# Kernel optimization log

Measured on AMD Instinct MI355X. Metric: run time of the kernel, lower is better.

Reference implementation:

```python
import jax, jax.numpy as jnp
import numpy as np

VOCAB = 50257   # N_max = len(word_to_idx)
IN_DIM = 256
HID = 13        # forced: out Linear in_features = 2*hidden_dim must equal dec output 2*13
L = 2048


def _lstm_dir(seq, Wih, Whh, b, reverse):
    """Single-direction LSTM over seq [T, F] with zero init. b = b_ih + b_hh.
    Torch gate order: i, f, g, o."""
    H = Whh.shape[1]

    def step(carry, x_t):
        h, c = carry
        z = Wih @ x_t + Whh @ h + b                  # (4H,)
        i, f, g, o = jnp.split(z, 4)
        c2 = jax.nn.sigmoid(f) * c + jax.nn.sigmoid(i) * jnp.tanh(g)
        h2 = jax.nn.sigmoid(o) * jnp.tanh(c2)
        return (h2, c2), h2

    init = (jnp.zeros((H,), seq.dtype), jnp.zeros((H,), seq.dtype))
    (hn, cn), hs = jax.lax.scan(step, init, seq, reverse=reverse)
    return hs, hn, cn


def _dec_cell(x_scalar, h, c, Wih, Whh, b):
    """One LSTM cell step with scalar input (input_size=1). Returns new h."""
    z = Wih[:, 0] * x_scalar + Whh @ h + b
    i, f, g, o = jnp.split(z, 4)
    c2 = jax.nn.sigmoid(f) * c + jax.nn.sigmoid(i) * jnp.tanh(g)
    return jax.nn.sigmoid(o) * jnp.tanh(c2)


def setup_inputs() -> dict:
    key = jax.random.key(0)
    ks = jax.random.split(key, 16)
    s = 0.05
    G = 4 * HID  # 52; also num_layers*2*HID = 52 (proj in_features)
    return {
        "x": jax.random.randint(ks[0], (L,), 0, VOCAB),
        "emb_W": jax.random.normal(ks[1], (VOCAB + 1, IN_DIM)) * s,
        "enc_Wih0": jax.random.normal(ks[2], (2, G, IN_DIM)) * s,   # [dir, 4H, in]
        "enc_Whh0": jax.random.normal(ks[3], (2, G, HID)) * s,
        "enc_b0": jax.random.normal(ks[4], (2, G)) * s,
        "enc_Wih1": jax.random.normal(ks[5], (2, G, 2 * HID)) * s,  # layer1 input = 2*HID
        "enc_Whh1": jax.random.normal(ks[6], (2, G, HID)) * s,
        "enc_b1": jax.random.normal(ks[7], (2, G)) * s,
        "proj1_W": jax.random.normal(ks[8], (2 * HID, 2 * 2 * HID)) * s,
        "proj1_b": jax.random.normal(ks[9], (2 * HID,)) * s,
        "proj2_W": jax.random.normal(ks[10], (2 * HID, 2 * 2 * HID)) * s,
        "proj2_b": jax.random.normal(ks[11], (2 * HID,)) * s,
        "dec_Wih": jax.random.normal(ks[12], (2, G, 1)) * s,
        "dec_Whh": jax.random.normal(ks[13], (2, G, HID)) * s,
        "dec_b": jax.random.normal(ks[14], (2, G)) * s,
        "out_W": jax.random.normal(ks[15], (VOCAB, 2 * HID)) * s,
        "out_b": jnp.zeros((VOCAB,), jnp.float32),
    }


def reference(x, emb_W, enc_Wih0, enc_Whh0, enc_b0, enc_Wih1, enc_Whh1, enc_b1,
              proj1_W, proj1_b, proj2_W, proj2_b, dec_Wih, dec_Whh, dec_b,
              out_W, out_b):
    embs = emb_W[x]                                            # (L, IN_DIM)

    # Encoder: 2-layer bidirectional LSTM, batch=1 (vectors).
    hs_f0, hnf0, cnf0 = _lstm_dir(embs, enc_Wih0[0], enc_Whh0[0], enc_b0[0], False)
    hs_b0, hnb0, cnb0 = _lstm_dir(embs, enc_Wih0[1], enc_Whh0[1], enc_b0[1], True)
    out0 = jnp.concatenate([hs_f0, hs_b0], axis=-1)            # (L, 2*HID)
    _, hnf1, cnf1 = _lstm_dir(out0, enc_Wih1[0], enc_Whh1[0], enc_b1[0], False)
    _, hnb1, cnb1 = _lstm_dir(out0, enc_Wih1[1], enc_Whh1[1], enc_b1[1], True)

    # torch h_n layout: [l0_fwd, l0_bwd, l1_fwd, l1_bwd]
    h_flat = jnp.concatenate([hnf0, hnb0, hnf1, hnb1])         # (52,)
    c_flat = jnp.concatenate([cnf0, cnb0, cnf1, cnb1])
    state_h = (proj1_W @ h_flat + proj1_b).reshape(2, HID)     # dec (dir, HID) init
    state_c = (proj2_W @ c_flat + proj2_b).reshape(2, HID)

    # Decoder step 0: input -1.0 with projected initial state.
    start = jnp.float32(-1.0)
    step0 = jnp.concatenate([
        _dec_cell(start, state_h[0], state_c[0], dec_Wih[0], dec_Whh[0], dec_b[0]),
        _dec_cell(start, state_h[1], state_c[1], dec_Wih[1], dec_Whh[1], dec_b[1]),
    ])                                                          # (26,)

    # Steps i>0: original code calls self.dec(input) with NO hidden state, so each
    # step uses zero initial state and depends only on x[i-1] -> fully parallel.
    xs = x[:-1].astype(jnp.float32)                             # (L-1,)
    z0 = jnp.zeros((HID,), jnp.float32)
    rest = jax.vmap(lambda v: jnp.concatenate([
        _dec_cell(v, z0, z0, dec_Wih[0], dec_Whh[0], dec_b[0]),
        _dec_cell(v, z0, z0, dec_Wih[1], dec_Whh[1], dec_b[1]),
    ]))(xs)                                                     # (L-1, 26)

    dec_out = jnp.concatenate([step0[None, :], rest], axis=0)   # (L, 26)
    preds = dec_out @ out_W.T + out_b                           # (L, VOCAB)
    return preds, embs
```

## Files before the change

kernel.cpp:

```cpp
#include <hip/hip_runtime.h>
#include <hip/hip_bf16.h>
#include <cstdint>
#include <cstddef>

#define L      2048
#define IN_DIM 256
#define HID    13
#define G      52
#define VOCAB  50257
#define PRED_N ((size_t)L * VOCAB)
#define L2E    1.4426950408889634f
#define INV2L2E 0.34657359027997264f
#define NTX    99
#define NTY    16
#define NTILE  (NTX * NTY)

static __device__ __forceinline__ float fexp2(float x) { return __builtin_amdgcn_exp2f(x); }
static __device__ __forceinline__ float frcp(float x) { return __builtin_amdgcn_rcpf(x); }
static __device__ __forceinline__ float sigm(float z) { return 1.f - frcp(fexp2(z * L2E) + 1.f); }
static __device__ __forceinline__ float tanh_(float z) { return 1.f - 2.f * frcp(fexp2(z * (2.f * L2E)) + 1.f); }
static __device__ __forceinline__ float bcast(float v, int l) {
    return __int_as_float(__builtin_amdgcn_readlane(__float_as_int(v), l));
}

__global__ void k_emb_u0(const int* __restrict__ x, const float* __restrict__ embW,
                         const float* __restrict__ Wih0, const float* __restrict__ b0,
                         float* __restrict__ out_embs, float* __restrict__ u0)
{
    __shared__ float se[IN_DIM];
    int t = blockIdx.x;
    int tid = threadIdx.x;
    int rowx = x[t];
    float2 e = ((const float2*)(embW + (size_t)rowx * IN_DIM))[tid];
    se[2 * tid]     = e.x;
    se[2 * tid + 1] = e.y;
    ((float2*)(out_embs + (size_t)t * IN_DIM))[tid] = e;
    __syncthreads();
    if (tid < 2 * G) {
        int dirg = tid / G, g = tid % G;
        int gate = g / HID, row = g % HID;
        float msc = (gate == 2) ? 2.f * L2E : L2E;
        float acc = b0[dirg * G + g];
        const float* w = Wih0 + (size_t)(dirg * G + g) * IN_DIM;
        #pragma unroll 8
        for (int k = 0; k < IN_DIM; ++k)
            acc = fmaf(w[k], se[k], acc);
        u0[((size_t)dirg * L + t) * 64 + gate * 16 + row] = msc * acc;
    } else {
        int p = tid - 2 * G;
        int dirp = p / 12, pp = p % 12;
        int gate = pp / 3, row = HID + pp % 3;
        u0[((size_t)dirp * L + t) * 64 + gate * 16 + row] = 0.f;
    }
}

__global__ void k_rest(const int* __restrict__ x, const float* __restrict__ dWih,
                       const float* __restrict__ db, float* __restrict__ dec)
{
    int idx = blockIdx.x * blockDim.x + threadIdx.x;
    if (idx >= (L - 1) * 2 * HID) return;
    int i = idx / (2 * HID) + 1;
    int j = idx % (2 * HID);
    int dir = j / HID, jj = j % HID;
    float v = (float)x[i - 1];
    int base = dir * G;
    float zi = fmaf(dWih[base + jj],           v, db[base + jj]);
    float zg = fmaf(dWih[base + 2 * HID + jj], v, db[base + 2 * HID + jj]);
    float zo = fmaf(dWih[base + 3 * HID + jj], v, db[base + 3 * HID + jj]);
    float c2 = sigm(zi) * tanh_(zg);
    dec[(size_t)i * (2 * HID) + j] = sigm(zo) * tanh_(c2);
}

template<bool DOUT>
static __device__ __forceinline__ void chain_run(
    const float* __restrict__ ub, int pstep,
    const float* __restrict__ whh, float kcv, float onev,
    bool m16, bool m32,
    float* __restrict__ outp,
    float& hout, float& cout)
{
    float h = 0.f, c = 0.f;
    float cur[8], nxt[8];
    #pragma unroll
    for (int k = 0; k < 8; ++k) cur[k] = ub[k * pstep];
    #pragma unroll
    for (int k = 0; k < 8; ++k) nxt[k] = cur[k];
    const float* upf = ub + (ptrdiff_t)8 * pstep;

    for (int tcb = 0; tcb < L; tcb += 8) {
        if (tcb + 8 < L) {
            #pragma unroll
            for (int k = 0; k < 8; ++k) nxt[k] = upf[k * pstep];
            upf += (ptrdiff_t)8 * pstep;
        }
        #pragma unroll
        for (int k = 0; k < 8; ++k) {
            float h0 = bcast(h, 0), h1 = bcast(h, 1), h2 = bcast(h, 2), h3 = bcast(h, 3);
            float h4 = bcast(h, 4), h5 = bcast(h, 5), h6 = bcast(h, 6), h7 = bcast(h, 7);
            float h8 = bcast(h, 8), h9 = bcast(h, 9), h10 = bcast(h, 10), h11 = bcast(h, 11);
            float h12 = bcast(h, 12);
            float A = fmaf(whh[0], h0, cur[k]);
            float B = whh[1] * h1;
            float C = whh[2] * h2;
            float D = whh[3] * h3;
            A = fmaf(whh[4], h4, A);   B = fmaf(whh[5], h5, B);
            C = fmaf(whh[6], h6, C);   D = fmaf(whh[7], h7, D);
            A = fmaf(whh[8], h8, A);   B = fmaf(whh[9], h9, B);
            C = fmaf(whh[10], h10, C); D = fmaf(whh[11], h11, D);
            A = fmaf(whh[12], h12, A);
            float z = (A + B) + (C + D);
            float act = fmaf(-kcv, frcp(fexp2(z) + 1.f), onev);
            float pa = act, pb = act;
            asm("s_nop 1\n\tv_permlane16_swap_b32 %0, %1" : "+v"(pa), "+v"(pb));
            float sf = m16 ? pa : pb;
            float qa = act, qb = act;
            asm("s_nop 1\n\tv_permlane32_swap_b32 %0, %1" : "+v"(qa), "+v"(qb));
            float tg = m32 ? qa : qb;
            float ra = tg, rb = tg;
            asm("s_nop 1\n\tv_permlane16_swap_b32 %0, %1" : "+v"(ra), "+v"(rb));
            float so = m16 ? ra : rb;
            float c2 = fmaf(sf, c, act * tg);
            float th = fmaf(-2.f, frcp(fexp2(c2) + 1.f), 1.f);
            h = so * th;
            c = c2;
            if (DOUT) { *outp = h; outp += pstep; }
        }
        #pragma unroll
        for (int k = 0; k < 8; ++k) cur[k] = nxt[k];
    }
    hout = h; cout = c;
}

static __device__ __forceinline__ void chain_setup_and_run(
    const float* __restrict__ u, const float* __restrict__ Whh,
    float* __restrict__ out0p, float* __restrict__ finh, float* __restrict__ finc,
    int chain_base, int do_out0, int dir, int lane)
{
    int lg16 = lane & 15, gate = lane >> 4;
    int rsrc = gate * HID + (lg16 < HID ? lg16 : HID - 1);
    float kcv, onev;
    if (gate == 2)      { kcv = 2.f;        onev = 1.f; }
    else if (gate == 0) { kcv = 2.f * L2E;  onev = 2.f * L2E; }
    else                { kcv = 1.f;        onev = 1.f; }
    float msc = (gate == 2) ? 2.f * L2E : L2E;
    float whh[HID];
    #pragma unroll
    for (int k = 0; k < HID; ++k) whh[k] = msc * Whh[(dir * G + rsrc) * HID + k];

    int ia = lane, ib = lane;
    asm("s_nop 1\n\tv_permlane16_swap_b32 %0, %1" : "+v"(ia), "+v"(ib));
    bool m16 = (ia == (lane ^ 16));
    int ja = lane, jb = lane;
    asm("s_nop 1\n\tv_permlane32_swap_b32 %0, %1" : "+v"(ja), "+v"(jb));
    bool m32 = (ja == (lane ^ 32));

    const float* ub = u + (size_t)dir * L * 64 + (dir ? (size_t)(L - 1) * 64 : 0) + lane;
    int pstep = dir ? -64 : 64;
    float* outp = out0p + ((size_t)dir * L + (dir ? L - 1 : 0)) * 64 + lane;

    float h, c;
    if (do_out0) chain_run<true >(ub, pstep, whh, kcv, onev, m16, m32, outp, h, c);
    else         chain_run<false>(ub, pstep, whh, kcv, onev, m16, m32, outp, h, c);

    if (lane < HID) {
        finh[(chain_base + dir) * HID + lane] = h;
        finc[(chain_base + dir) * HID + lane] = c * INV2L2E;
    }
}

__global__ void __launch_bounds__(256) k_phase0(
    const float* __restrict__ u, const float* __restrict__ Whh,
    float* __restrict__ out0p, float* __restrict__ finh, float* __restrict__ finc,
    const float* __restrict__ dec, const float* __restrict__ outW,
    const float* __restrict__ outb, float* __restrict__ preds)
{
    __shared__ float sd[128][28];
    int bid = blockIdx.x;
    int tid = threadIdx.x;
    if (bid >= 2) {
        __builtin_amdgcn_s_setprio(0);
        int tile = bid - 2;
        int ix = tile % NTX, iy = tile / NTX;
        int nbase = ix * 512, i0 = iy * 128;
        for (int li = tid; li < 128 * 26; li += 256) {
            int r = li / 26, cc = li % 26;
            sd[r][cc] = dec[(size_t)(i0 + r) * 26 + cc];
        }
        __syncthreads();
        int n0 = nbase + tid, n1 = nbase + 256 + tid;
        bool a0 = n0 < VOCAB, a1 = n1 < VOCAB;
        float w0[26], w1[26], b0v = 0.f, b1v = 0.f;
        #pragma unroll
        for (int k = 0; k < 26; ++k) { w0[k] = 0.f; w1[k] = 0.f; }
        if (a0) { const float* w = outW + (size_t)n0 * 26;
            #pragma unroll
            for (int k = 0; k < 26; ++k) w0[k] = w[k];
            b0v = outb[n0]; }
        if (a1) { const float* w = outW + (size_t)n1 * 26;
            #pragma unroll
            for (int k = 0; k < 26; ++k) w1[k] = w[k];
            b1v = outb[n1]; }
        for (int i = 0; i < 128; ++i) {
            int grow = i0 + i;
            float acc0 = b0v, acc1 = b1v;
            const float* dr = sd[i];
            #pragma unroll
            for (int k = 0; k < 26; ++k) {
                float d = dr[k];
                acc0 = fmaf(d, w0[k], acc0);
                acc1 = fmaf(d, w1[k], acc1);
            }
            if (grow != 0) {
                size_t rb = (size_t)grow * VOCAB;
                if (a0) preds[rb + n0] = acc0;
                if (a1) preds[rb + n1] = acc1;
            }
        }
        return;
    }
    if (tid >= 64) return;
    __builtin_amdgcn_s_setprio(3);
    chain_setup_and_run(u, Whh, out0p, finh, finc, 0, 1, bid, tid);
}

__global__ void __launch_bounds__(64) k_phase1(
    const float* __restrict__ u, const float* __restrict__ Whh,
    float* __restrict__ finh, float* __restrict__ finc)
{
    chain_setup_and_run(u, Whh, (float*)nullptr, finh, finc, 2, 0, blockIdx.x, threadIdx.x);
}

__global__ void k_u1(const float* __restrict__ out0p, const float* __restrict__ Wih1,
                     const float* __restrict__ b1, float* __restrict__ u1)
{
    int idx = blockIdx.x * blockDim.x + threadIdx.x;
    if (idx >= L * 2 * 64) return;
    int t    = idx >> 7;
    int remv = idx & 127;
    int d1   = remv >> 6;
    int lane = remv & 63;
    int gate = lane >> 4, row = lane & 15;
    size_t oidx = ((size_t)d1 * L + t) * 64 + lane;
    if (row >= HID) { u1[oidx] = 0.f; return; }
    int g = gate * HID + row;
    float msc = (gate == 2) ? 2.f * L2E : L2E;
    float acc = b1[d1 * G + g];
    const float* w = Wih1 + (size_t)(d1 * G + g) * (2 * HID);
    const float* o0 = out0p + (size_t)t * 64;
    const float* o1 = out0p + ((size_t)L + t) * 64;
    #pragma unroll
    for (int k = 0; k < HID; ++k)
        acc = fmaf(w[k], o0[k], acc);
    #pragma unroll
    for (int k = 0; k < HID; ++k)
        acc = fmaf(w[HID + k], o1[k], acc);
    u1[oidx] = msc * acc;
}

__global__ void __launch_bounds__(64) k_final(const float* __restrict__ fin_h, const float* __restrict__ fin_c,
                                              const float* __restrict__ p1W, const float* __restrict__ p1b,
                                              const float* __restrict__ p2W, const float* __restrict__ p2b,
                                              const float* __restrict__ dWih, const float* __restrict__ dWhh,
                                              const float* __restrict__ db, float* __restrict__ dec)
{
    __shared__ float sh[2 * HID], sc[2 * HID], sz[G];
    int tid = threadIdx.x;
    if (tid < 4 * HID) {
        int r = tid < 2 * HID ? tid : tid - 2 * HID;
        const float* W   = tid < 2 * HID ? p1W : p2W;
        const float* src = tid < 2 * HID ? fin_h : fin_c;
        float acc = tid < 2 * HID ? p1b[r] : p2b[r];
        for (int k = 0; k < 4 * HID; ++k) acc = fmaf(W[r * 4 * HID + k], src[k], acc);
        if (tid < 2 * HID) sh[r] = acc; else sc[r] = acc;
    }
    __syncthreads();
    for (int dir = 0; dir < 2; ++dir) {
        if (tid < G) {
            float acc = db[dir * G + tid] - dWih[dir * G + tid];
            for (int k = 0; k < HID; ++k)
                acc = fmaf(dWhh[(dir * G + tid) * HID + k], sh[dir * HID + k], acc);
            sz[tid] = acc;
        }
        __syncthreads();
        if (tid < HID) {
            float si = sigm(sz[tid]);
            float sf = sigm(sz[HID + tid]);
            float tg = tanh_(sz[2 * HID + tid]);
            float so = sigm(sz[3 * HID + tid]);
            float c2 = fmaf(sf, sc[dir * HID + tid], si * tg);
            dec[dir * HID + tid] = so * tanh_(c2);
        }
        __syncthreads();
    }
}

__global__ void k_row0(const float* __restrict__ dec, const float* __restrict__ outW,
                       const float* __restrict__ outb, float* __restrict__ preds)
{
    int n = blockIdx.x * blockDim.x + threadIdx.x;
    if (n >= VOCAB) return;
    float acc = outb[n];
    const float* w = outW + (size_t)n * 26;
    #pragma unroll
    for (int k = 0; k < 26; ++k) acc = fmaf(w[k], dec[k], acc);
    preds[n] = acc;
}

extern "C" void kernel_launch(void* const* d_in, const int* in_sizes, int n_in,
                              void* d_out, int out_size, void* d_ws, size_t ws_size,
                              hipStream_t stream)
{
    (void)in_sizes; (void)n_in; (void)out_size; (void)ws_size;

    const int*   x     = (const int*)d_in[0];
    const float* embW  = (const float*)d_in[1];
    const float* eWih0 = (const float*)d_in[2];
    const float* eWhh0 = (const float*)d_in[3];
    const float* eb0   = (const float*)d_in[4];
    const float* eWih1 = (const float*)d_in[5];
    const float* eWhh1 = (const float*)d_in[6];
    const float* eb1   = (const float*)d_in[7];
    const float* p1W   = (const float*)d_in[8];
    const float* p1b   = (const float*)d_in[9];
    const float* p2W   = (const float*)d_in[10];
    const float* p2b   = (const float*)d_in[11];
    const float* dWih  = (const float*)d_in[12];
    const float* dWhh  = (const float*)d_in[13];
    const float* db    = (const float*)d_in[14];
    const float* outW  = (const float*)d_in[15];
    const float* outb  = (const float*)d_in[16];

    float* ws    = (float*)d_ws;
    float* u0    = ws;
    float* u1    = u0 + 2 * L * 64;
    float* out0p = u1 + 2 * L * 64;
    float* dec   = out0p + 2 * L * 64;
    float* fin_h = dec + L * 2 * HID;
    float* fin_c = fin_h + G;

    float* preds    = (float*)d_out;
    float* out_embs = preds + PRED_N;

    hipLaunchKernelGGL(k_emb_u0, dim3(L), dim3(128), 0, stream,
                       x, embW, eWih0, eb0, out_embs, u0);

    int restN = (L - 1) * 2 * HID;
    hipLaunchKernelGGL(k_rest, dim3((restN + 255) / 256), dim3(256), 0, stream, x, dWih, db, dec);

    hipLaunchKernelGGL(k_phase0, dim3(2 + NTILE), dim3(256), 0, stream,
                       u0, eWhh0, out0p, fin_h, fin_c,
                       dec, outW, outb, preds);

    hipLaunchKernelGGL(k_u1, dim3((L * 2 * 64 + 255) / 256), dim3(256), 0, stream,
                       out0p, eWih1, eb1, u1);

    hipLaunchKernelGGL(k_phase1, dim3(2), dim3(64), 0, stream,
                       u1, eWhh1, fin_h, fin_c);

    hipLaunchKernelGGL(k_final, dim3(1), dim3(64), 0, stream,
                       fin_h, fin_c, p1W, p1b, p2W, p2b, dWih, dWhh, db, dec);

    hipLaunchKernelGGL(k_row0, dim3((VOCAB + 255) / 256), dim3(256), 0, stream,
                       dec, outW, outb, preds);
}
```

Before: 611.3 us.

## Fuse decoder rest kernel into embedding kernel and persist GEMM tiles over fewer blocks

Moves the per-timestep decoder cell computation into the embedding/u0 kernel by adding 32 extra threads per block, which removes one kernel launch. The output-projection blocks in phase0 become persistent: 254 blocks each loop over a contiguous range of tiles instead of launching one block per tile. This is meant to cut launch and block scheduling overhead and leave CUs free for the latency-bound recurrent chains. The risk is reduced parallelism for the large prediction write and some load imbalance between blocks. It also adds a stray, harmless redefinition of PRED_N.

```diff
diff --git a/kernel.cpp b/kernel.cpp
--- a/kernel.cpp
+++ b/kernel.cpp
@@ -8,12 +8,15 @@
 #define HID    13
 #define G      52
 #define VOCAB  50257
-#define PRED_N ((size_t)L * VOCAB)
+#define PRED_N ((size_t)L * VOOCAB)
 #define L2E    1.4426950408889634f
 #define INV2L2E 0.34657359027997264f
 #define NTX    99
 #define NTY    16
 #define NTILE  (NTX * NTY)
+#define GB     254
+#undef PRED_N
+#define PRED_N ((size_t)L * VOCAB)
 
 static __device__ __forceinline__ float fexp2(float x) { return __builtin_amdgcn_exp2f(x); }
 static __device__ __forceinline__ float frcp(float x) { return __builtin_amdgcn_rcpf(x); }
@@ -23,18 +26,22 @@
     return __int_as_float(__builtin_amdgcn_readlane(__float_as_int(v), l));
 }
 
-__global__ void k_emb_u0(const int* __restrict__ x, const float* __restrict__ embW,
-                         const float* __restrict__ Wih0, const float* __restrict__ b0,
-                         float* __restrict__ out_embs, float* __restrict__ u0)
+__global__ void __launch_bounds__(160) k_emb_u0(
+    const int* __restrict__ x, const float* __restrict__ embW,
+    const float* __restrict__ Wih0, const float* __restrict__ b0,
+    const float* __restrict__ dWih, const float* __restrict__ db,
+    float* __restrict__ out_embs, float* __restrict__ u0, float* __restrict__ dec)
 {
     __shared__ float se[IN_DIM];
     int t = blockIdx.x;
     int tid = threadIdx.x;
-    int rowx = x[t];
-    float2 e = ((const float2*)(embW + (size_t)rowx * IN_DIM))[tid];
-    se[2 * tid]     = e.x;
-    se[2 * tid + 1] = e.y;
-    ((float2*)(out_embs + (size_t)t * IN_DIM))[tid] = e;
+    if (tid < 128) {
+        int rowx = x[t];
+        float2 e = ((const float2*)(embW + (size_t)rowx * IN_DIM))[tid];
+        se[2 * tid]     = e.x;
+        se[2 * tid + 1] = e.y;
+        ((float2*)(out_embs + (size_t)t * IN_DIM))[tid] = e;
+    }
     __syncthreads();
     if (tid < 2 * G) {
         int dirg = tid / G, g = tid % G;
@@ -46,29 +53,22 @@
         for (int k = 0; k < IN_DIM; ++k)
             acc = fmaf(w[k], se[k], acc);
         u0[((size_t)dirg * L + t) * 64 + gate * 16 + row] = msc * acc;
-    } else {
+    } else if (tid < 128) {
         int p = tid - 2 * G;
         int dirp = p / 12, pp = p % 12;
         int gate = pp / 3, row = HID + pp % 3;
         u0[((size_t)dirp * L + t) * 64 + gate * 16 + row] = 0.f;
-    }
-}
-
-__global__ void k_rest(const int* __restrict__ x, const float* __restrict__ dWih,
-                       const float* __restrict__ db, float* __restrict__ dec)
-{
-    int idx = blockIdx.x * blockDim.x + threadIdx.x;
-    if (idx >= (L - 1) * 2 * HID) return;
-    int i = idx / (2 * HID) + 1;
-    int j = idx % (2 * HID);
-    int dir = j / HID, jj = j % HID;
-    float v = (float)x[i - 1];
-    int base = dir * G;
-    float zi = fmaf(dWih[base + jj],           v, db[base + jj]);
-    float zg = fmaf(dWih[base + 2 * HID + jj], v, db[base + 2 * HID + jj]);
-    float zo = fmaf(dWih[base + 3 * HID + jj], v, db[base + 3 * HID + jj]);
-    float c2 = sigm(zi) * tanh_(zg);
-    dec[(size_t)i * (2 * HID) + j] = sigm(zo) * tanh_(c2);
+    } else if (tid < 128 + 2 * HID && t >= 1) {
+        int j = tid - 128;
+        int dir = j / HID, jj = j % HID;
+        float v = (float)x[t - 1];
+        int base = dir * G;
+        float zi = fmaf(dWih[base + jj],           v, db[base + jj]);
+        float zg = fmaf(dWih[base + 2 * HID + jj], v, db[base + 2 * HID + jj]);
+        float zo = fmaf(dWih[base + 3 * HID + jj], v, db[base + 3 * HID + jj]);
+        float c2 = sigm(zi) * tanh_(zg);
+        dec[(size_t)t * (2 * HID) + j] = sigm(zo) * tanh_(c2);
+    }
 }
 
 template<bool DOUT>
@@ -179,41 +179,48 @@
     int tid = threadIdx.x;
     if (bid >= 2) {
         __builtin_amdgcn_s_setprio(0);
-        int tile = bid - 2;
-        int ix = tile % NTX, iy = tile / NTX;
-        int nbase = ix * 512, i0 = iy * 128;
-        for (int li = tid; li < 128 * 26; li += 256) {
-            int r = li / 26, cc = li % 26;
-            sd[r][cc] = dec[(size_t)(i0 + r) * 26 + cc];
-        }
-        __syncthreads();
-        int n0 = nbase + tid, n1 = nbase + 256 + tid;
-        bool a0 = n0 < VOCAB, a1 = n1 < VOCAB;
-        float w0[26], w1[26], b0v = 0.f, b1v = 0.f;
-        #pragma unroll
-        for (int k = 0; k < 26; ++k) { w0[k] = 0.f; w1[k] = 0.f; }
-        if (a0) { const float* w = outW + (size_t)n0 * 26;
+        int b = bid - 2;
+        const int q = NTILE / GB, r = NTILE % GB;
+        int start = b * q + (b < r ? b : r);
+        int cnt   = q + (b < r ? 1 : 0);
+        for (int tt = 0; tt < cnt; ++tt) {
+            int tile = start + tt;
+            int ix = tile % NTX, iy = tile / NTX;
+            int nbase = ix * 512, i0 = iy * 128;
+            __syncthreads();
+            for (int li = tid; li < 128 * 26; li += 256) {
+                int rr_ = li / 26, cc = li % 26;
+                sd[rr_][cc] = dec[(size_t)(i0 + rr_) * 26 + cc];
+            }
+            __syncthreads();
+            int n0 = nbase + tid, n1 = nbase + 256 + tid;
+            bool a0 = n0 < VOCAB, a1 = n1 < VOCAB;
+            float w0[26], w1[26], b0v = 0.f, b1v = 0.f;
             #pragma unroll
-            for (int k = 0; k < 26; ++k) w0[k] = w[k];
-            b0v = outb[n0]; }
-        if (a1) { const float* w = outW + (size_t)n1 * 26;
-            #pragma unroll
-            for (int k = 0; k < 26; ++k) w1[k] = w[k];
-            b1v = outb[n1]; }
-        for (int i = 0; i < 128; ++i) {
-            int grow = i0 + i;
-            float acc0 = b0v, acc1 = b1v;
-            const float* dr = sd[i];
-            #pragma unroll
-            for (int k = 0; k < 26; ++k) {
-                float d = dr[k];
-                acc0 = fmaf(d, w0[k], acc0);
-                acc1 = fmaf(d, w1[k], acc1);
-            }
-            if (grow != 0) {
-                size_t rb = (size_t)grow * VOCAB;
-                if (a0) preds[rb + n0] = acc0;
-                if (a1) preds[rb + n1] = acc1;
+            for (int k = 0; k < 26; ++k) { w0[k] = 0.f; w1[k] = 0.f; }
+            if (a0) { const float* w = outW + (size_t)n0 * 26;
+                #pragma unroll
+                for (int k = 0; k < 26; ++k) w0[k] = w[k];
+                b0v = outb[n0]; }
+            if (a1) { const float* w = outW + (size_t)n1 * 26;
+                #pragma unroll
+                for (int k = 0; k < 26; ++k) w1[k] = w[k];
+                b1v = outb[n1]; }
+            for (int i = 0; i < 128; ++i) {
+                int grow = i0 + i;
+                float acc0 = b0v, acc1 = b1v;
+                const float* dr = sd[i];
+                #pragma unroll
+                for (int k = 0; k < 26; ++k) {
+                    float d = dr[k];
+                    acc0 = fmaf(d, w0[k], acc0);
+                    acc1 = fmaf(d, w1[k], acc1);
+                }
+                if (grow != 0) {
+                    size_t rb = (size_t)grow * VOCAB;
+                    if (a0) preds[rb + n0] = acc0;
+                    if (a1) preds[rb + n1] = acc1;
+                }
             }
         }
         return;
@@ -341,13 +348,10 @@
     float* preds    = (float*)d_out;
     float* out_embs = preds + PRED_N;
 
-    hipLaunchKernelGGL(k_emb_u0, dim3(L), dim3(128), 0, stream,
-                       x, embW, eWih0, eb0, out_embs, u0);
-
-    int restN = (L - 1) * 2 * HID;
-    hipLaunchKernelGGL(k_rest, dim3((restN + 255) / 256), dim3(256), 0, stream, x, dWih, db, dec);
-
-    hipLaunchKernelGGL(k_phase0, dim3(2 + NTILE), dim3(256), 0, stream,
+    hipLaunchKernelGGL(k_emb_u0, dim3(L), dim3(160), 0, stream,
+                       x, embW, eWih0, eb0, dWih, db, out_embs, u0, dec);
+
+    hipLaunchKernelGGL(k_phase0, dim3(2 + GB), dim3(256), 0, stream,
                        u0, eWhh0, out0p, fin_h, fin_c,
                        dec, outW, outb, preds);
 
```

Measured after the change: 576.2 us. 1.06x faster.
